# Optimization experiments

Measured on AMD Instinct MI355X. Metric: run time of the kernel, lower is better.

## Reference

```python
import jax, jax.numpy as jnp
import numpy as np

B, S, D, L, V = 2, 1024, 1024, 8, 32000
EPS = 1e-8


def rmsnorm(x, w):
    return x * jax.lax.rsqrt(jnp.mean(x * x, axis=-1, keepdims=True) + EPS) * w


def lerp_scan(v, a):
    # h_t = (1 - a_t) * h_{t-1} + a_t * v_t over time axis=1 (h_0 = 0)
    A = 1.0 - a
    Bv = a * v
    def comb(l, r):
        return (l[0] * r[0], l[1] * r[0] + r[1])
    _, h = jax.lax.associative_scan(comb, (A, Bv), axis=1)
    return h


def mrt_layer(x, kw, cw, cb, w1, b1, w2, b2, nw):
    res = x @ kw                                   # [B,S,2D]
    theta, alpha = jnp.split(res, 2, axis=-1)
    h = lerp_scan(jnp.tanh(theta) * jnp.pi, jax.nn.sigmoid(alpha))  # [B,S,D]
    # causal depthwise conv, kernel 3, manual left pad of 2
    hc = jnp.pad(h.transpose(0, 2, 1), ((0, 0), (0, 0), (2, 0)))    # [B,D,S+2]
    hb = jax.lax.conv_general_dilated(
        hc, cw, window_strides=(1,), padding='VALID',
        dimension_numbers=('NCH', 'OIH', 'NCH'), feature_group_count=D)
    hb = (hb + cb[None, :, None]).transpose(0, 2, 1)                # [B,S,D]
    z = h + hb
    hf = jax.nn.silu(z @ w1 + b1) @ w2 + b2
    return rmsnorm(hf, nw)


def setup_inputs() -> dict:
    key = jax.random.key(0)
    ks = jax.random.split(key, 10)
    s = 0.02
    return {
        'input_ids': jax.random.randint(ks[0], (B, S), 0, V),
        'embedding': jax.random.normal(ks[1], (V, D), dtype=jnp.float32) * 0.002,
        'pos_emb': jax.random.normal(ks[2], (1, 1024, D), dtype=jnp.float32) * 0.002,
        'keygen_w': jax.random.normal(ks[3], (L, D, 2 * D), dtype=jnp.float32) * s,
        'conv_w': jax.random.normal(ks[4], (L, D, 1, 3), dtype=jnp.float32) * s,
        'conv_b': jnp.zeros((L, D), dtype=jnp.float32),
        'mlp_w1': jax.random.normal(ks[5], (L, D, 2 * D), dtype=jnp.float32) * s,
        'mlp_b1': jnp.zeros((L, 2 * D), dtype=jnp.float32),
        'mlp_w2': jax.random.normal(ks[6], (L, 2 * D, D), dtype=jnp.float32) * s,
        'mlp_b2': jnp.zeros((L, D), dtype=jnp.float32),
        'norm_w': jnp.ones((L, D), dtype=jnp.float32),
        'plastic': jnp.zeros((4, D, D), dtype=jnp.float32),
        'final_norm_w': jnp.ones((D,), dtype=jnp.float32),
    }


def reference(input_ids, embedding, pos_emb, keygen_w, conv_w, conv_b,
              mlp_w1, mlp_b1, mlp_w2, mlp_b2, norm_w, plastic, final_norm_w):
    seq = input_ids.shape[1]
    x = embedding[input_ids] + pos_emb[:, :seq, :]
    x = x / jnp.maximum(jnp.linalg.norm(x, axis=-1, keepdims=True), 1e-12)  # F.normalize
    for i in range(L):
        delta = mrt_layer(x, keygen_w[i], conv_w[i], conv_b[i],
                          mlp_w1[i], mlp_b1[i], mlp_w2[i], mlp_b2[i], norm_w[i])
        if i >= L - 4:
            x = x + delta + delta @ plastic[i - (L - 4)]
        else:
            x = x + delta
    x = rmsnorm(x, final_norm_w)
    # eval mode: dropout is identity
    x = x * jax.lax.rsqrt(jnp.mean(x * x, axis=-1, keepdims=True) + 1e-8) * 0.8
    logits = x @ embedding.T                       # tied lm_head
    std = jnp.std(logits, axis=-1, keepdims=True, ddof=1)  # torch.std unbiased
    logits = logits / jnp.maximum(std, 1.0)
    return jnp.clip(logits, -10.0, 10.0)
```

## Files before the change

### kernel.cpp

```cpp
#include <hip/hip_runtime.h>


using short8 = __attribute__((ext_vector_type(8))) short;
using half8  = __attribute__((ext_vector_type(8))) _Float16;
using f32x4  = __attribute__((ext_vector_type(4))) float;

#define DEVI __device__ __forceinline__

DEVI float sigm(float x) { return 1.0f / (1.0f + expf(-x)); }

DEVI float block_sum256(float v) {
  #pragma unroll
  for (int o = 32; o > 0; o >>= 1) v += __shfl_down(v, o, 64);
  __shared__ float sm[4];
  if ((threadIdx.x & 63) == 0) sm[threadIdx.x >> 6] = v;
  __syncthreads();
  float t = sm[0] + sm[1] + sm[2] + sm[3];
  __syncthreads();
  return t;
}

DEVI void gload16(const void* g, void* l) {
  __builtin_amdgcn_global_load_lds(
      (const __attribute__((address_space(1))) unsigned*)g,
      (__attribute__((address_space(3))) unsigned*)l, 16, 0, 0);
}

__global__ __launch_bounds__(512, 2) void gemm12h(
    const _Float16* __restrict__ A, const _Float16* __restrict__ B,
    int M, int N, int K,
    float* __restrict__ outF, float* __restrict__ psum, float* __restrict__ psq)
{
  __shared__ __align__(16) unsigned short lds[2][2][256 * 32];
  const int tid  = threadIdx.x;
  const int lane = tid & 63, wid = tid >> 6;
  const int wr = wid >> 2, wc = wid & 3;
  const int myr = lane & 15;
  const int kq  = lane >> 4;

  const int nwg  = gridDim.x;
  const int flat = blockIdx.x;
  const int swz  = (flat & 7) * (nwg >> 3) + (flat >> 3);
  const int MT   = M >> 8;
  const int m0   = (swz % MT) * 256;
  const int nt   = swz / MT;
  const int n0   = nt * 256;
  const int NT   = K / 32;

  auto stage = [&](int b, int k0) {
    #pragma unroll
    for (int q = 0; q < 2; ++q) {
      const int row  = q * 128 + wid * 16 + (lane >> 2);
      const int scol = ((lane & 3) ^ ((row >> 1) & 3)) << 3;
      const int lb   = (q * 128 + wid * 16) * 32;
      gload16(A + (size_t)(m0 + row) * K + k0 + scol, &lds[b][0][lb]);
      gload16(B + (size_t)(n0 + row) * K + k0 + scol, &lds[b][1][lb]);
    }
  };

  f32x4 acc[8][4] = {};

  stage(0, 0);
  stage(1, 32);
  for (int t = 0; t < NT; ++t) {
    const int b = t & 1;
    if (t + 1 < NT) { asm volatile("s_waitcnt vmcnt(4)" ::: "memory"); }
    else            { asm volatile("s_waitcnt vmcnt(0)" ::: "memory"); }
    __builtin_amdgcn_s_barrier();
    asm volatile("" ::: "memory");

    short8 af[8], bf[4];
    #pragma unroll
    for (int i = 0; i < 8; ++i) {
      const int ra = wr * 128 + i * 16 + myr;
      af[i] = *(const short8*)&lds[b][0][ra * 32 + ((kq ^ ((ra >> 1) & 3)) << 3)];
    }
    #pragma unroll
    for (int j = 0; j < 4; ++j) {
      const int rb = wc * 64 + j * 16 + myr;
      bf[j] = *(const short8*)&lds[b][1][rb * 32 + ((kq ^ ((rb >> 1) & 3)) << 3)];
    }
    asm volatile("s_waitcnt lgkmcnt(0)" ::: "memory");
    __builtin_amdgcn_s_barrier();
    asm volatile("" ::: "memory");
    if (t + 2 < NT) stage(b, (t + 2) * 32);
    __builtin_amdgcn_sched_barrier(0);
    __builtin_amdgcn_s_setprio(1);
    #pragma unroll
    for (int i = 0; i < 8; ++i)
      #pragma unroll
      for (int j = 0; j < 4; ++j)
        acc[i][j] = __builtin_amdgcn_mfma_f32_16x16x32_f16(
            __builtin_bit_cast(half8, af[i]), __builtin_bit_cast(half8, bf[j]),
            acc[i][j], 0, 0, 0);
    __builtin_amdgcn_s_setprio(0);
  }

  #pragma unroll
  for (int i8 = 0; i8 < 8; ++i8) {
    const int rbase = m0 + wr * 128 + i8 * 16 + (kq << 2);
    #pragma unroll
    for (int j4 = 0; j4 < 4; ++j4) {
      const int col = n0 + wc * 64 + j4 * 16 + myr;
      #pragma unroll
      for (int r = 0; r < 4; ++r)
        outF[(size_t)(rbase + r) * N + col] = acc[i8][j4][r];
    }
  }

  const int PW = N >> 6;
  const int pcol = (n0 >> 6) + wc;
  #pragma unroll
  for (int i8 = 0; i8 < 8; ++i8)
    #pragma unroll
    for (int r = 0; r < 4; ++r) {
      float s = 0.f, ss = 0.f;
      #pragma unroll
      for (int j4 = 0; j4 < 4; ++j4) {
        float v = acc[i8][j4][r];
        s += v; ss += v * v;
      }
      #pragma unroll
      for (int mk = 1; mk < 16; mk <<= 1) {
        s  += __shfl_xor(s,  mk, 64);
        ss += __shfl_xor(ss, mk, 64);
      }
      if (myr == ((i8 * 4 + r) & 15)) {
        const int row = m0 + wr * 128 + i8 * 16 + kq * 4 + r;
        psum[(size_t)row * PW + pcol] = s;
        psq [(size_t)row * PW + pcol] = ss;
      }
    }
}

template<int EPI, int KSPLIT>
__global__ __launch_bounds__(512, 2) void gemm13(
    const _Float16* __restrict__ A, const _Float16* __restrict__ B,
    int M, int N, int K,
    float* __restrict__ outF, _Float16* __restrict__ outH,
    const float* __restrict__ bias, int halfN)
{
  __shared__ __align__(16) unsigned short lds[2][2][128 * 64];
  const int tid  = threadIdx.x;
  const int lane = tid & 63, wid = tid >> 6;
  const int wr = wid >> 2, wc = wid & 3;
  const int myr = lane & 15;
  const int kq  = lane >> 4;

  const int nwg  = gridDim.x;
  const int flat = blockIdx.x;
  const int swz  = (flat & 7) * (nwg >> 3) + (flat >> 3);
  const int ks   = (KSPLIT > 1) ? (swz % KSPLIT) : 0;
  const int tile = (KSPLIT > 1) ? (swz / KSPLIT) : swz;
  const int MT   = M >> 7;
  const int m0   = (tile % MT) * 128;
  const int n0   = (tile / MT) * 128;
  const int Kc   = K / KSPLIT;
  const int kbase = ks * Kc;
  const int NT   = Kc / 64;

  auto stage = [&](int b, int k0) {
    #pragma unroll
    for (int q = 0; q < 2; ++q) {
      const int row  = q * 64 + wid * 8 + (lane >> 3);
      const int scol = ((lane & 7) ^ (row & 7)) << 3;
      const int lb   = (q * 64 + wid * 8) * 64;
      gload16(A + (size_t)(m0 + row) * K + k0 + scol, &lds[b][0][lb]);
      gload16(B + (size_t)(n0 + row) * K + k0 + scol, &lds[b][1][lb]);
    }
  };

  f32x4 acc[4][2] = {};

  stage(0, kbase);
  stage(1, kbase + 64);
  for (int t = 0; t < NT; ++t) {
    const int b = t & 1;
    if (t + 1 < NT) { asm volatile("s_waitcnt vmcnt(4)" ::: "memory"); }
    else            { asm volatile("s_waitcnt vmcnt(0)" ::: "memory"); }
    __builtin_amdgcn_s_barrier();
    asm volatile("" ::: "memory");

    #pragma unroll
    for (int kk = 0; kk < 2; ++kk) {
      short8 af[4], bf[2];
      #pragma unroll
      for (int i = 0; i < 4; ++i) {
        const int ra = wr * 64 + i * 16 + myr;
        af[i] = *(const short8*)&lds[b][0][ra * 64 + (((kk * 4 + kq) ^ (ra & 7)) << 3)];
      }
      #pragma unroll
      for (int j = 0; j < 2; ++j) {
        const int rb = wc * 32 + j * 16 + myr;
        bf[j] = *(const short8*)&lds[b][1][rb * 64 + (((kk * 4 + kq) ^ (rb & 7)) << 3)];
      }
      asm volatile("s_waitcnt lgkmcnt(0)" ::: "memory");
      if (kk == 1) {
        __builtin_amdgcn_s_barrier();
        asm volatile("" ::: "memory");
        if (t + 2 < NT) stage(b, kbase + (t + 2) * 64);
      }
      __builtin_amdgcn_sched_barrier(0);
      __builtin_amdgcn_s_setprio(1);
      #pragma unroll
      for (int i = 0; i < 4; ++i)
        #pragma unroll
        for (int j = 0; j < 2; ++j)
          acc[i][j] = __builtin_amdgcn_mfma_f32_16x16x32_f16(
              __builtin_bit_cast(half8, af[i]), __builtin_bit_cast(half8, bf[j]),
              acc[i][j], 0, 0, 0);
      __builtin_amdgcn_s_setprio(0);
    }
  }

  const size_t MN = (size_t)M * N;
  #pragma unroll
  for (int i = 0; i < 4; ++i) {
    const int rbase = m0 + wr * 64 + i * 16 + (kq << 2);
    #pragma unroll
    for (int j = 0; j < 2; ++j) {
      const int col = n0 + wc * 32 + j * 16 + myr;
      if constexpr (EPI == 1) {
        f32x4 v;
        #pragma unroll
        for (int r = 0; r < 4; ++r) {
          float c = acc[i][j][r];
          v[r] = (col < halfN) ? (tanhf(c) * 3.14159265358979323846f) : sigm(c);
        }
        *(f32x4*)&outF[(size_t)col * M + rbase] = v;
      } else {
        #pragma unroll
        for (int r = 0; r < 4; ++r) {
          float c = acc[i][j][r];
          const size_t idx = (size_t)(rbase + r) * N + col;
          if constexpr (EPI == 2) {
            c += bias[col];
            outH[idx] = (_Float16)(c * sigm(c));
          } else if constexpr (EPI == 4) {
            float xn = outF[idx] + c;
            outF[idx] = xn;
            outH[idx] = (_Float16)xn;
          } else if constexpr (EPI == 5) {
            outF[(size_t)ks * MN + idx] = c;
          }
        }
      }
    }
  }
}

__global__ __launch_bounds__(256) void scanconv(
    const float* __restrict__ vaT, const float* __restrict__ cw,
    const float* __restrict__ cb, _Float16* __restrict__ z16,
    int S, int D, int M)
{
  const int dl = threadIdx.x & 7;
  const int c  = threadIdx.x >> 3;
  const int ch = blockIdx.x * 8 + dl;
  const int b = ch >> 10, d = ch & 1023;
  const float* vrow = vaT + (size_t)d * M + b * S;
  const float* arow = vaT + (size_t)(D + d) * M + b * S;
  const int s0 = c * 32;

  f32x4 vr[8], ar[8];
  float A = 1.f, Bv = 0.f, Apm = 1.f, Bpm = 0.f;
  #pragma unroll
  for (int t = 0; t < 8; ++t) {
    vr[t] = *(const f32x4*)&vrow[s0 + t * 4];
    ar[t] = *(const f32x4*)&arow[s0 + t * 4];
    #pragma unroll
    for (int r = 0; r < 4; ++r) {
      if (t * 4 + r == 31) { Apm = A; Bpm = Bv; }
      float na = 1.f - ar[t][r];
      A *= na;
      Bv = Bv * na + ar[t][r] * vr[t][r];
    }
  }
  __shared__ float Asm[32][9], Bsm[32][9], Aps[32][9], Bps[32][9];
  Asm[c][dl] = A; Bsm[c][dl] = Bv; Aps[c][dl] = Apm; Bps[c][dl] = Bpm;
  __syncthreads();
  if (threadIdx.x < 8) {
    float run = 0.f;
    for (int cc = 0; cc < 32; ++cc) {
      float A_ = Asm[cc][dl], B_ = Bsm[cc][dl];
      Bsm[cc][dl] = run;
      run = A_ * run + B_;
    }
  }
  __syncthreads();
  float hm1 = Bsm[c][dl];
  float hm2 = (c == 0) ? 0.f
            : (Aps[c - 1][dl] * Bsm[c - 1][dl] + Bps[c - 1][dl]);

  const float w0 = cw[d * 3 + 0], w1 = cw[d * 3 + 1], w2 = cw[d * 3 + 2];
  const float bc = cb[d];
  #pragma unroll
  for (int t = 0; t < 8; ++t) {
    #pragma unroll
    for (int r = 0; r < 4; ++r) {
      float h = hm1 + ar[t][r] * (vr[t][r] - hm1);
      float z = h + bc + w0 * hm2 + w1 * hm1 + w2 * h;
      z16[(size_t)(b * S + s0 + t * 4 + r) * D + d] = (_Float16)z;
      hm2 = hm1; hm1 = h;
    }
  }
}

__global__ __launch_bounds__(256) void rms_fuse(
    const float* __restrict__ p, const float* __restrict__ bias,
    const float* __restrict__ nw, float* __restrict__ x,
    _Float16* __restrict__ o16, int D, int mode, size_t MN)
{
  const size_t base = (size_t)blockIdx.x * D;
  float vloc[4]; float ss = 0.f;
  #pragma unroll
  for (int q = 0; q < 4; ++q) {
    int d = threadIdx.x + q * 256;
    float v = p[base + d] + p[MN + base + d] + bias[d];
    vloc[q] = v; ss += v * v;
  }
  ss = block_sum256(ss);
  float r = 1.f / sqrtf(ss / D + 1e-8f);
  #pragma unroll
  for (int q = 0; q < 4; ++q) {
    int d = threadIdx.x + q * 256;
    float delta = vloc[q] * r * nw[d];
    float xn = x[base + d] + delta;
    x[base + d] = xn;
    o16[base + d] = (_Float16)(mode ? delta : xn);
  }
}

__global__ __launch_bounds__(256) void embed_norm(
    const int* __restrict__ ids, const float* __restrict__ emb,
    const float* __restrict__ pos,
    float* __restrict__ x, _Float16* __restrict__ x16, int S, int D)
{
  const int rowi = blockIdx.x;
  const int s = rowi % S;
  const int tok = ids[rowi];
  const size_t eb = (size_t)tok * D, pb = (size_t)s * D, xb = (size_t)rowi * D;
  float vloc[4]; float ss = 0.f;
  #pragma unroll
  for (int q = 0; q < 4; ++q) {
    int d = threadIdx.x + q * 256;
    float v = emb[eb + d] + pos[pb + d];
    vloc[q] = v; ss += v * v;
  }
  ss = block_sum256(ss);
  float r = 1.f / fmaxf(sqrtf(ss), 1e-12f);
  #pragma unroll
  for (int q = 0; q < 4; ++q) {
    int d = threadIdx.x + q * 256;
    float v = vloc[q] * r;
    x[xb + d] = v;
    x16[xb + d] = (_Float16)v;
  }
}

__global__ __launch_bounds__(256) void final_norm(
    const float* __restrict__ x, const float* __restrict__ w,
    _Float16* __restrict__ xf, int D)
{
  const size_t base = (size_t)blockIdx.x * D;
  float s1 = 0.f, s2 = 0.f;
  float vloc[4], wloc[4];
  #pragma unroll
  for (int q = 0; q < 4; ++q) {
    int d = threadIdx.x + q * 256;
    float v = x[base + d], ww = w[d];
    vloc[q] = v; wloc[q] = ww;
    s1 += v * v; s2 += v * ww * v * ww;
  }
  s1 = block_sum256(s1);
  s2 = block_sum256(s2);
  float r1 = 1.f / sqrtf(s1 / D + 1e-8f);
  float m2 = r1 * r1 * (s2 / D);
  float r2 = 1.f / sqrtf(m2 + 1e-8f);
  float sc = r1 * r2 * 0.8f;
  #pragma unroll
  for (int q = 0; q < 4; ++q) {
    int d = threadIdx.x + q * 256;
    xf[base + d] = (_Float16)(vloc[q] * wloc[q] * sc);
  }
}

__global__ __launch_bounds__(256) void fix_row(
    float* __restrict__ out, const float* __restrict__ psum,
    const float* __restrict__ psq, int PW, int V)
{
  const int row = blockIdx.x;
  float s = 0.f, q = 0.f;
  for (int j = threadIdx.x; j < PW; j += 256) {
    s += psum[(size_t)row * PW + j];
    q += psq [(size_t)row * PW + j];
  }
  s = block_sum256(s);
  q = block_sum256(q);
  float mean = s / V;
  float var = (q - (float)V * mean * mean) / (float)(V - 1);
  var = fmaxf(var, 0.f);
  const float sc = 1.f / fmaxf(sqrtf(var), 1.f);
  float* rowp = out + (size_t)row * V;
  for (int j = threadIdx.x * 4; j < V; j += 1024) {
    f32x4 v = *(f32x4*)&rowp[j];
    #pragma unroll
    for (int t = 0; t < 4; ++t)
      v[t] = fminf(fmaxf(v[t] * sc, -10.f), 10.f);
    *(f32x4*)&rowp[j] = v;
  }
}

__global__ void tsplit16(const float* __restrict__ W, _Float16* __restrict__ WT,
                         int K, int N)
{
  __shared__ float t[32][33];
  const size_t bo = (size_t)blockIdx.z * K * N;
  const int tx = threadIdx.x, ty = threadIdx.y;
  #pragma unroll
  for (int i = 0; i < 32; i += 8) {
    int kk = blockIdx.y * 32 + ty + i;
    int nn = blockIdx.x * 32 + tx;
    t[ty + i][tx] = W[bo + (size_t)kk * N + nn];
  }
  __syncthreads();
  #pragma unroll
  for (int i = 0; i < 32; i += 8) {
    int nn = blockIdx.x * 32 + ty + i;
    int kk = blockIdx.y * 32 + tx;
    WT[bo + (size_t)nn * K + kk] = (_Float16)t[tx][ty + i];
  }
}

__global__ void cvt_f16(const float* __restrict__ in, _Float16* __restrict__ o, size_t n)
{
  for (size_t i = (size_t)blockIdx.x * 256 + threadIdx.x; i < n;
       i += (size_t)gridDim.x * 256)
    o[i] = (_Float16)in[i];
}

extern "C" void kernel_launch(void* const* d_in, const int* in_sizes, int n_in,
                              void* d_out, int out_size, void* d_ws, size_t ws_size,
                              hipStream_t stream)
{
  (void)in_sizes; (void)n_in; (void)out_size; (void)ws_size;
  const int*   ids = (const int*)  d_in[0];
  const float* emb = (const float*)d_in[1];
  const float* pos = (const float*)d_in[2];
  const float* kw  = (const float*)d_in[3];
  const float* cw  = (const float*)d_in[4];
  const float* cb  = (const float*)d_in[5];
  const float* w1  = (const float*)d_in[6];
  const float* b1  = (const float*)d_in[7];
  const float* w2  = (const float*)d_in[8];
  const float* b2  = (const float*)d_in[9];
  const float* nw  = (const float*)d_in[10];
  const float* pl  = (const float*)d_in[11];
  const float* fnw = (const float*)d_in[12];
  float* out = (float*)d_out;

  constexpr int B = 2, S = 1024, D = 1024, L = 8, V = 32000;
  constexpr int M = B * S;
  const size_t MN = (size_t)M * D;

  size_t off = 0;
  auto alloc = [&](size_t bytes) {
    char* p = (char*)d_ws + off;
    off += (bytes + 255) & ~(size_t)255;
    return (void*)p;
  };
  _Float16* kwT  = (_Float16*)alloc((size_t)L * 2 * D * D * 2);
  _Float16* w1T  = (_Float16*)alloc((size_t)L * 2 * D * D * 2);
  _Float16* w2T  = (_Float16*)alloc((size_t)L * 2 * D * D * 2);
  _Float16* plT  = (_Float16*)alloc((size_t)4 * D * D * 2);
  _Float16* emb16 = (_Float16*)alloc((size_t)V * D * 2);
  float* x    = (float*)alloc(MN * 4);
  _Float16* x16 = (_Float16*)alloc(MN * 2);
  float* vaT  = (float*)alloc((size_t)M * 2 * D * 4);
  float* pbig = (float*)alloc(2 * MN * 4);
  _Float16* z16 = (_Float16*)alloc(MN * 2);
  _Float16* u16 = (_Float16*)alloc((size_t)M * 2 * D * 2);
  _Float16* d16 = (_Float16*)alloc(MN * 2);
  _Float16* xf16 = (_Float16*)alloc(MN * 2);

  const int PW = V >> 6;
  float* psum = vaT;
  float* psq  = vaT + (size_t)M * PW;

  {
    dim3 tb(32, 8);
    tsplit16<<<dim3(2 * D / 32, D / 32, L), tb, 0, stream>>>(kw, kwT, D, 2 * D);
    tsplit16<<<dim3(2 * D / 32, D / 32, L), tb, 0, stream>>>(w1, w1T, D, 2 * D);
    tsplit16<<<dim3(D / 32, 2 * D / 32, L), tb, 0, stream>>>(w2, w2T, 2 * D, D);
    tsplit16<<<dim3(D / 32, D / 32, 4),     tb, 0, stream>>>(pl, plT, D, D);
    cvt_f16<<<4096, 256, 0, stream>>>(emb, emb16, (size_t)V * D);
  }

  embed_norm<<<M, 256, 0, stream>>>(ids, emb, pos, x, x16, S, D);

  for (int i = 0; i < L; ++i) {
    const _Float16* kwi = kwT + (size_t)i * 2 * D * D;
    const _Float16* w1i = w1T + (size_t)i * 2 * D * D;
    const _Float16* w2i = w2T + (size_t)i * 2 * D * D;

    gemm13<1, 1><<<(M / 128) * (2 * D / 128), 512, 0, stream>>>(
        x16, kwi, M, 2 * D, D, vaT, nullptr, nullptr, D);

    scanconv<<<B * D / 8, 256, 0, stream>>>(
        vaT, cw + (size_t)i * D * 3, cb + (size_t)i * D, z16, S, D, M);

    gemm13<2, 1><<<(M / 128) * (2 * D / 128), 512, 0, stream>>>(
        z16, w1i, M, 2 * D, D, nullptr, u16, b1 + (size_t)i * 2 * D, 0);

    gemm13<5, 2><<<(M / 128) * (D / 128) * 2, 512, 0, stream>>>(
        u16, w2i, M, D, 2 * D, pbig, nullptr, nullptr, 0);

    const int mode = (i >= L - 4) ? 1 : 0;
    rms_fuse<<<M, 256, 0, stream>>>(pbig, b2 + (size_t)i * D, nw + (size_t)i * D,
                                    x, mode ? d16 : x16, D, mode, MN);
    if (mode) {
      const _Float16* pli = plT + (size_t)(i - 4) * D * D;
      gemm13<4, 1><<<(M / 128) * (D / 128), 512, 0, stream>>>(
          d16, pli, M, D, D, x, x16, nullptr, 0);
    }
  }

  final_norm<<<M, 256, 0, stream>>>(x, fnw, xf16, D);

  gemm12h<<<(M / 256) * (V / 256), 512, 0, stream>>>(
      xf16, emb16, M, V, D, out, psum, psq);

  fix_row<<<M, 256, 0, stream>>>(out, psum, psq, PW, V);
}
```

Baseline: 1.076 ms.

## Store GEMM intermediates in fp16 and move the stage barrier after both k-steps

The keygen GEMM now writes its tanh/sigmoid outputs as fp16, and the split-K W2 GEMM writes fp16 partials. The scan-conv and RMS-fuse kernels read these fp16 buffers, halving the intermediate memory traffic. The GEMM main loop also moves the LDS wait, the barrier and the next-tile staging to after both kk sub-steps, removing the per-kk lgkmcnt wait and sched_barrier. Risks are lost precision in the scan inputs and split-K partials, and less overlap of the staging loads with MFMA work.

```diff
diff --git a/kernel.cpp b/kernel.cpp
--- a/kernel.cpp
+++ b/kernel.cpp
@@ -3,6 +3,7 @@
 
 using short8 = __attribute__((ext_vector_type(8))) short;
 using half8  = __attribute__((ext_vector_type(8))) _Float16;
+using half4  = __attribute__((ext_vector_type(4))) _Float16;
 using f32x4  = __attribute__((ext_vector_type(4))) float;
 
 #define DEVI __device__ __forceinline__
@@ -134,7 +135,7 @@
 }
 
 template<int EPI, int KSPLIT>
-__global__ __launch_bounds__(512, 2) void gemm13(
+__global__ __launch_bounds__(512, 2) void gemm16(
     const _Float16* __restrict__ A, const _Float16* __restrict__ B,
     int M, int N, int K,
     float* __restrict__ outF, _Float16* __restrict__ outH,
@@ -194,13 +195,6 @@
         const int rb = wc * 32 + j * 16 + myr;
         bf[j] = *(const short8*)&lds[b][1][rb * 64 + (((kk * 4 + kq) ^ (rb & 7)) << 3)];
       }
-      asm volatile("s_waitcnt lgkmcnt(0)" ::: "memory");
-      if (kk == 1) {
-        __builtin_amdgcn_s_barrier();
-        asm volatile("" ::: "memory");
-        if (t + 2 < NT) stage(b, kbase + (t + 2) * 64);
-      }
-      __builtin_amdgcn_sched_barrier(0);
       __builtin_amdgcn_s_setprio(1);
       #pragma unroll
       for (int i = 0; i < 4; ++i)
@@ -211,6 +205,11 @@
               acc[i][j], 0, 0, 0);
       __builtin_amdgcn_s_setprio(0);
     }
+
+    asm volatile("s_waitcnt lgkmcnt(0)" ::: "memory");
+    __builtin_amdgcn_s_barrier();
+    asm volatile("" ::: "memory");
+    if (t + 2 < NT) stage(b, kbase + (t + 2) * 64);
   }
 
   const size_t MN = (size_t)M * N;
@@ -221,13 +220,14 @@
     for (int j = 0; j < 2; ++j) {
       const int col = n0 + wc * 32 + j * 16 + myr;
       if constexpr (EPI == 1) {
-        f32x4 v;
+        half4 hv;
         #pragma unroll
         for (int r = 0; r < 4; ++r) {
           float c = acc[i][j][r];
-          v[r] = (col < halfN) ? (tanhf(c) * 3.14159265358979323846f) : sigm(c);
+          hv[r] = (_Float16)((col < halfN) ? (tanhf(c) * 3.14159265358979323846f)
+                                           : sigm(c));
         }
-        *(f32x4*)&outF[(size_t)col * M + rbase] = v;
+        *(half4*)&outH[(size_t)col * M + rbase] = hv;
       } else {
         #pragma unroll
         for (int r = 0; r < 4; ++r) {
@@ -241,7 +241,7 @@
             outF[idx] = xn;
             outH[idx] = (_Float16)xn;
           } else if constexpr (EPI == 5) {
-            outF[(size_t)ks * MN + idx] = c;
+            outH[(size_t)ks * MN + idx] = (_Float16)c;
           }
         }
       }
@@ -250,7 +250,7 @@
 }
 
 __global__ __launch_bounds__(256) void scanconv(
-    const float* __restrict__ vaT, const float* __restrict__ cw,
+    const _Float16* __restrict__ vaT, const float* __restrict__ cw,
     const float* __restrict__ cb, _Float16* __restrict__ z16,
     int S, int D, int M)
 {
@@ -258,18 +258,20 @@
   const int c  = threadIdx.x >> 3;
   const int ch = blockIdx.x * 8 + dl;
   const int b = ch >> 10, d = ch & 1023;
-  const float* vrow = vaT + (size_t)d * M + b * S;
-  const float* arow = vaT + (size_t)(D + d) * M + b * S;
+  const _Float16* vrow = vaT + (size_t)d * M + b * S;
+  const _Float16* arow = vaT + (size_t)(D + d) * M + b * S;
   const int s0 = c * 32;
 
   f32x4 vr[8], ar[8];
   float A = 1.f, Bv = 0.f, Apm = 1.f, Bpm = 0.f;
   #pragma unroll
   for (int t = 0; t < 8; ++t) {
-    vr[t] = *(const f32x4*)&vrow[s0 + t * 4];
-    ar[t] = *(const f32x4*)&arow[s0 + t * 4];
+    half4 v4 = *(const half4*)&vrow[s0 + t * 4];
+    half4 a4 = *(const half4*)&arow[s0 + t * 4];
     #pragma unroll
     for (int r = 0; r < 4; ++r) {
+      vr[t][r] = (float)v4[r];
+      ar[t][r] = (float)a4[r];
       if (t * 4 + r == 31) { Apm = A; Bpm = Bv; }
       float na = 1.f - ar[t][r];
       A *= na;
@@ -307,7 +309,7 @@
 }
 
 __global__ __launch_bounds__(256) void rms_fuse(
-    const float* __restrict__ p, const float* __restrict__ bias,
+    const _Float16* __restrict__ p, const float* __restrict__ bias,
     const float* __restrict__ nw, float* __restrict__ x,
     _Float16* __restrict__ o16, int D, int mode, size_t MN)
 {
@@ -316,7 +318,7 @@
   #pragma unroll
   for (int q = 0; q < 4; ++q) {
     int d = threadIdx.x + q * 256;
-    float v = p[base + d] + p[MN + base + d] + bias[d];
+    float v = (float)p[base + d] + (float)p[MN + base + d] + bias[d];
     vloc[q] = v; ss += v * v;
   }
   ss = block_sum256(ss);
@@ -476,16 +478,16 @@
   _Float16* emb16 = (_Float16*)alloc((size_t)V * D * 2);
   float* x    = (float*)alloc(MN * 4);
   _Float16* x16 = (_Float16*)alloc(MN * 2);
-  float* vaT  = (float*)alloc((size_t)M * 2 * D * 4);
-  float* pbig = (float*)alloc(2 * MN * 4);
+  _Float16* vaT16 = (_Float16*)alloc((size_t)M * 2 * D * 2);
+  _Float16* p16   = (_Float16*)alloc(2 * MN * 2);
   _Float16* z16 = (_Float16*)alloc(MN * 2);
   _Float16* u16 = (_Float16*)alloc((size_t)M * 2 * D * 2);
   _Float16* d16 = (_Float16*)alloc(MN * 2);
   _Float16* xf16 = (_Float16*)alloc(MN * 2);
+  float* psum = (float*)alloc((size_t)M * (V >> 6) * 4);
+  float* psq  = (float*)alloc((size_t)M * (V >> 6) * 4);
 
   const int PW = V >> 6;
-  float* psum = vaT;
-  float* psq  = vaT + (size_t)M * PW;
 
   {
     dim3 tb(32, 8);
@@ -503,24 +505,24 @@
     const _Float16* w1i = w1T + (size_t)i * 2 * D * D;
     const _Float16* w2i = w2T + (size_t)i * 2 * D * D;
 
-    gemm13<1, 1><<<(M / 128) * (2 * D / 128), 512, 0, stream>>>(
-        x16, kwi, M, 2 * D, D, vaT, nullptr, nullptr, D);
+    gemm16<1, 1><<<(M / 128) * (2 * D / 128), 512, 0, stream>>>(
+        x16, kwi, M, 2 * D, D, nullptr, vaT16, nullptr, D);
 
     scanconv<<<B * D / 8, 256, 0, stream>>>(
-        vaT, cw + (size_t)i * D * 3, cb + (size_t)i * D, z16, S, D, M);
-
-    gemm13<2, 1><<<(M / 128) * (2 * D / 128), 512, 0, stream>>>(
+        vaT16, cw + (size_t)i * D * 3, cb + (size_t)i * D, z16, S, D, M);
+
+    gemm16<2, 1><<<(M / 128) * (2 * D / 128), 512, 0, stream>>>(
         z16, w1i, M, 2 * D, D, nullptr, u16, b1 + (size_t)i * 2 * D, 0);
 
-    gemm13<5, 2><<<(M / 128) * (D / 128) * 2, 512, 0, stream>>>(
-        u16, w2i, M, D, 2 * D, pbig, nullptr, nullptr, 0);
+    gemm16<5, 2><<<(M / 128) * (D / 128) * 2, 512, 0, stream>>>(
+        u16, w2i, M, D, 2 * D, nullptr, p16, nullptr, 0);
 
     const int mode = (i >= L - 4) ? 1 : 0;
-    rms_fuse<<<M, 256, 0, stream>>>(pbig, b2 + (size_t)i * D, nw + (size_t)i * D,
+    rms_fuse<<<M, 256, 0, stream>>>(p16, b2 + (size_t)i * D, nw + (size_t)i * D,
                                     x, mode ? d16 : x16, D, mode, MN);
     if (mode) {
       const _Float16* pli = plT + (size_t)(i - 4) * D * D;
-      gemm13<4, 1><<<(M / 128) * (D / 128), 512, 0, stream>>>(
+      gemm16<4, 1><<<(M / 128) * (D / 128), 512, 0, stream>>>(
           d16, pli, M, D, D, x, x16, nullptr, 0);
     }
   }
```

Measured after the change: 1.040 ms. -3.3%, faster.
